# Kernel tuning notes

Hardware: AMD Instinct MI355X
Metric: run time of the kernel (lower is better)

The kernel has to match this reference:

```python
import jax, jax.numpy as jnp
import numpy as np

D = 1024
H = 16
HD = D // H


def setup_inputs() -> dict:
    key = jax.random.key(0)
    ks = jax.random.split(key, 11)
    B, S = 4, 1024
    s = 0.02
    return {
        "q": jax.random.normal(ks[0], (B, S, D), jnp.float32),
        "k": jax.random.normal(ks[1], (B, S, D), jnp.float32),
        "v": jax.random.normal(ks[2], (B, S, D), jnp.float32),
        "Wq": jax.random.normal(ks[3], (D, D), jnp.float32) * s,
        "bq": jnp.zeros((D,), jnp.float32),
        "Wk": jax.random.normal(ks[4], (D, D), jnp.float32) * s,
        "bk": jnp.zeros((D,), jnp.float32),
        "Wv": jax.random.normal(ks[5], (D, D), jnp.float32) * s,
        "bv": jnp.zeros((D,), jnp.float32),
        "Wo": jax.random.normal(ks[6], (D, D), jnp.float32) * s,
        "bo": jnp.zeros((D,), jnp.float32),
    }


def _split_heads(x):
    # [B, S, D] -> [B, H, S, HD]
    B, S, _ = x.shape
    return x.reshape(B, S, H, HD).transpose(0, 2, 1, 3)


def reference(q, k, v, Wq, bq, Wk, bk, Wv, bv, Wo, bo):
    # Projections followed by ReLU (faithful to the original module)
    qh = _split_heads(jax.nn.relu(q @ Wq + bq))
    kh = _split_heads(jax.nn.relu(k @ Wk + bk))
    vh = _split_heads(jax.nn.relu(v @ Wv + bv))
    # NOTE: original scales by sqrt(input_dim), not sqrt(head_dim)
    scale = 1.0 / jnp.sqrt(jnp.float32(D))
    scores = jnp.einsum("bhsd,bhtd->bhst", qh, kh) * scale  # [B,H,S,S]
    weights = jax.nn.softmax(scores, axis=-1)  # dropout is identity in eval
    attn = jnp.einsum("bhst,bhtd->bhsd", weights, vh)  # [B,H,S,HD]
    B, _, S, _ = attn.shape
    attn = attn.transpose(0, 2, 1, 3).reshape(B, S, D)
    return attn @ Wo + bo
```

## Files before the change

### kernel.cpp

```cpp
#include <hip/hip_runtime.h>
#include <math.h>

#define Dm 1024
#define Hn 16
#define HDn 64
#define Sn 1024

typedef __attribute__((ext_vector_type(8))) __bf16 bf16x8;
typedef __attribute__((ext_vector_type(4))) float floatx4;

__device__ __forceinline__ void async_ld16(void* lds, const void* g) {
    __builtin_amdgcn_global_load_lds(
        (const __attribute__((address_space(1))) void*)g,
        (__attribute__((address_space(3))) void*)lds,
        16, 0, 0);
}

struct PrepArgs {
    const float* qkv[3];
    __bf16*      qkv_o[3];
    const float* W[4];
    __bf16*      WT[4];
    float*       out_zero;
};

__global__ __launch_bounds__(256) void prep_kernel(PrepArgs a)
{
    __shared__ float sT[64][65];
    const int z = blockIdx.z, x = blockIdx.x, tid = threadIdx.x;

    if (z < 3) {
        const float* src = a.qkv[z];
        __bf16* dst = a.qkv_o[z];
        const int lin = x * 256 + tid;
        const float4 v0 = ((const float4*)src)[lin * 2];
        const float4 v1 = ((const float4*)src)[lin * 2 + 1];
        bf16x8 o;
        o[0] = (__bf16)v0.x; o[1] = (__bf16)v0.y; o[2] = (__bf16)v0.z; o[3] = (__bf16)v0.w;
        o[4] = (__bf16)v1.x; o[5] = (__bf16)v1.y; o[6] = (__bf16)v1.z; o[7] = (__bf16)v1.w;
        ((bf16x8*)dst)[lin] = o;
    } else if (z < 7) {
        if (x >= 256) return;
        const float* W = a.W[z - 3];
        __bf16* O = a.WT[z - 3];
        const int bi = (x >> 4) * 64, bj = (x & 15) * 64;
        const int colr = tid & 63, rowg = tid >> 6;
        #pragma unroll
        for (int i = 0; i < 16; ++i) {
            const int kk = i * 4 + rowg;
            sT[kk][colr] = W[(size_t)(bi + kk) * Dm + bj + colr];
        }
        __syncthreads();
        #pragma unroll
        for (int i = 0; i < 16; ++i) {
            const int rn = i * 4 + rowg;
            O[(size_t)(bj + rn) * Dm + bi + colr] = (__bf16)sT[colr][rn];
        }
    } else {
        float4* o = (float4*)a.out_zero;
        const int i = (x * 256 + tid) * 2;
        const float4 zz = make_float4(0.f, 0.f, 0.f, 0.f);
        o[i] = zz;
        o[i + 1] = zz;
    }
}

struct GemmArgs {
    const __bf16* X[3];
    const __bf16* WT[3];
    const float*  bias[3];
    void*         out[3];
    int   layout[3];
    float esc[3];
};

__global__ __launch_bounds__(256) void gemm_bf16_kernel(GemmArgs args)
{
    __shared__ __align__(16) __bf16 sA[128 * 32];
    __shared__ __align__(16) __bf16 sB[128 * 32];

    const int z = blockIdx.z;
    const __bf16* __restrict__ Xb  = args.X[z];
    const __bf16* __restrict__ WTb = args.WT[z];
    const float*  __restrict__ bias = args.bias[z];
    void* __restrict__ outp = args.out[z];
    const int layout = args.layout[z];
    const float escale = args.esc[z];

    const int tid = threadIdx.x;
    const int id = blockIdx.x + (blockIdx.y << 3);
    const int bm = (((id & 7) << 2) | (id >> 6)) * 128;
    const int bn = ((id >> 3) & 7) * 128;

    const int lane = tid & 63;
    const int wave = tid >> 6;
    const int wm = (wave & 1) * 64;
    const int wn = (wave >> 1) * 64;
    const int l15 = lane & 15, quad = lane >> 4;

    floatx4 acc[4][4];
    #pragma unroll
    for (int mi = 0; mi < 4; ++mi)
        #pragma unroll
        for (int ni = 0; ni < 4; ++ni)
            acc[mi][ni] = (floatx4){0.f, 0.f, 0.f, 0.f};

    const int cA0 = tid,       p0 = cA0 >> 3, g0 = (cA0 & 7) ^ (p0 & 7);
    const int cA1 = tid + 256, p1 = cA1 >> 3, g1 = (cA1 & 7) ^ (p1 & 7);
    const int r0 = 2 * p0 + (g0 >> 2), q0 = g0 & 3;
    const int r1 = 2 * p1 + (g1 >> 2), q1 = g1 & 3;
    const __bf16* gA0 = Xb  + (size_t)(bm + r0) * Dm + q0 * 8;
    const __bf16* gA1 = Xb  + (size_t)(bm + r1) * Dm + q1 * 8;
    const __bf16* gB0 = WTb + (size_t)(bn + r0) * Dm + q0 * 8;
    const __bf16* gB1 = WTb + (size_t)(bn + r1) * Dm + q1 * 8;
    char* const lA0 = (char*)sA + (tid & 192) * 16;
    char* const lA1 = (char*)sA + (256 + (tid & 192)) * 16;
    char* const lB0 = (char*)sB + (tid & 192) * 16;
    char* const lB1 = (char*)sB + (256 + (tid & 192)) * 16;

    int offA[4], offB[4];
    #pragma unroll
    for (int mi = 0; mi < 4; ++mi) {
        const int r = wm + mi * 16 + l15;
        const int p = r >> 1;
        const int cc = ((((r & 1) << 2) | quad)) ^ (p & 7);
        offA[mi] = p * 64 + cc * 8;
    }
    #pragma unroll
    for (int ni = 0; ni < 4; ++ni) {
        const int r = wn + ni * 16 + l15;
        const int p = r >> 1;
        const int cc = ((((r & 1) << 2) | quad)) ^ (p & 7);
        offB[ni] = p * 64 + cc * 8;
    }

    for (int kt = 0; kt < Dm; kt += 32) {
        async_ld16(lA0, gA0 + kt);
        async_ld16(lA1, gA1 + kt);
        async_ld16(lB0, gB0 + kt);
        async_ld16(lB1, gB1 + kt);
        __syncthreads();

        bf16x8 af[4], bfr[4];
        #pragma unroll
        for (int mi = 0; mi < 4; ++mi) af[mi] = *(const bf16x8*)(sA + offA[mi]);
        #pragma unroll
        for (int ni = 0; ni < 4; ++ni) bfr[ni] = *(const bf16x8*)(sB + offB[ni]);
        #pragma unroll
        for (int mi = 0; mi < 4; ++mi)
            #pragma unroll
            for (int ni = 0; ni < 4; ++ni)
                acc[mi][ni] = __builtin_amdgcn_mfma_f32_16x16x32_bf16(
                    af[mi], bfr[ni], acc[mi][ni], 0, 0, 0);
        __syncthreads();
    }

    #pragma unroll
    for (int mi = 0; mi < 4; ++mi) {
        #pragma unroll
        for (int ni = 0; ni < 4; ++ni) {
            const int n = bn + wn + ni * 16 + l15;
            const float bv = bias[n];
            const int h = n >> 6, d = n & 63;
            #pragma unroll
            for (int reg = 0; reg < 4; ++reg) {
                const int m = bm + wm + mi * 16 + quad * 4 + reg;
                const int b = m >> 10, s = m & 1023;
                float v = fmaxf(acc[mi][ni][reg] + bv, 0.0f) * escale;
                if (layout == 0)
                    ((__bf16*)outp)[((size_t)(b * Hn + h) * 1024 + s) * 64 + d] = (__bf16)v;
                else
                    ((__bf16*)outp)[((size_t)(b * Hn + h) * 64 + d) * 1024 + s] = (__bf16)v;
            }
        }
    }
}

__global__ __launch_bounds__(256) void gemm_splitk_kernel(
    const __bf16* __restrict__ Xb, const __bf16* __restrict__ WTb,
    const float* __restrict__ bias, float* __restrict__ outp)
{
    __shared__ __align__(16) __bf16 sA[128 * 64];
    __shared__ __align__(16) __bf16 sB[128 * 64];

    const int tid = threadIdx.x;
    const int kz = blockIdx.z;
    const int id = blockIdx.x + (blockIdx.y << 3);
    const int bm = (((id & 7) << 2) | (id >> 6)) * 128;
    const int bn = ((id >> 3) & 7) * 128;

    const int lane = tid & 63;
    const int wave = tid >> 6;
    const int wm = (wave & 1) * 64;
    const int wn = (wave >> 1) * 64;
    const int l15 = lane & 15, quad = lane >> 4;

    floatx4 acc[4][4];
    #pragma unroll
    for (int mi = 0; mi < 4; ++mi)
        #pragma unroll
        for (int ni = 0; ni < 4; ++ni)
            acc[mi][ni] = (floatx4){0.f, 0.f, 0.f, 0.f};

    const int kofs = kz * 512;
    const __bf16* gA[4];
    const __bf16* gB[4];
    #pragma unroll
    for (int j = 0; j < 4; ++j) {
        const int c = j * 256 + tid;
        const int row = c >> 3;
        const int q = (c & 7) ^ (row & 7);
        gA[j] = Xb  + (size_t)(bm + row) * Dm + kofs + q * 8;
        gB[j] = WTb + (size_t)(bn + row) * Dm + kofs + q * 8;
    }
    char* const lA = (char*)sA + (tid & 192) * 16;
    char* const lB = (char*)sB + (tid & 192) * 16;

    for (int kt = 0; kt < 512; kt += 64) {
        #pragma unroll
        for (int j = 0; j < 4; ++j) {
            async_ld16(lA + j * 4096, gA[j] + kt);
            async_ld16(lB + j * 4096, gB[j] + kt);
        }
        __syncthreads();

        #pragma unroll
        for (int ks = 0; ks < 2; ++ks) {
            bf16x8 af[4], bfr[4];
            #pragma unroll
            for (int mi = 0; mi < 4; ++mi) {
                const int r = wm + mi * 16 + l15;
                af[mi] = *(const bf16x8*)(sA + r * 64 + ((((ks << 2) + quad) ^ (r & 7)) * 8));
            }
            #pragma unroll
            for (int ni = 0; ni < 4; ++ni) {
                const int r = wn + ni * 16 + l15;
                bfr[ni] = *(const bf16x8*)(sB + r * 64 + ((((ks << 2) + quad) ^ (r & 7)) * 8));
            }
            #pragma unroll
            for (int mi = 0; mi < 4; ++mi)
                #pragma unroll
                for (int ni = 0; ni < 4; ++ni)
                    acc[mi][ni] = __builtin_amdgcn_mfma_f32_16x16x32_bf16(
                        af[mi], bfr[ni], acc[mi][ni], 0, 0, 0);
        }
        __syncthreads();
    }

    #pragma unroll
    for (int mi = 0; mi < 4; ++mi) {
        #pragma unroll
        for (int ni = 0; ni < 4; ++ni) {
            const int n = bn + wn + ni * 16 + l15;
            const float bv = (kz == 0) ? bias[n] : 0.0f;
            #pragma unroll
            for (int reg = 0; reg < 4; ++reg) {
                const int m = bm + wm + mi * 16 + quad * 4 + reg;
                atomicAdd(outp + (size_t)m * 1024 + n, acc[mi][ni][reg] + bv);
            }
        }
    }
}

__global__ __launch_bounds__(256, 2) void flash_attn_kernel(
    const __bf16* __restrict__ Qh,
    const __bf16* __restrict__ Kh,
    const __bf16* __restrict__ Vt,
    __bf16* __restrict__ ctx)
{
    __shared__ __align__(16) char sKV[2][16384];
    __shared__ __align__(16) __bf16 sP[4][32 * 64];

    const int tid = threadIdx.x;
    const int wave = tid >> 6, lane = tid & 63;
    const int l15 = lane & 15, quad = lane >> 4;

    const int id = blockIdx.x + (blockIdx.y << 3) + (blockIdx.z << 7);
    const int kk = id >> 3;
    const int bh = ((id & 7) << 3) | (kk & 7);
    const int b = bh >> 4, h = bh & 15;
    const int qb = (kk >> 3) * 128 + wave * 32;

    bf16x8 aQ[2][2];
    #pragma unroll
    for (int mi = 0; mi < 2; ++mi)
        #pragma unroll
        for (int ks = 0; ks < 2; ++ks)
            aQ[mi][ks] = *(const bf16x8*)(Qh +
                (size_t)(bh * Sn + qb + mi * 16 + l15) * 64 + ks * 32 + quad * 8);

    const int s0 = tid, s1 = tid + 256;
    const int r0 = s0 >> 3, q0c = (s0 & 7) ^ (r0 & 7);
    const int r1 = s1 >> 3, q1c = (s1 & 7) ^ (r1 & 7);
    const __bf16* gK0 = Kh + (size_t)(bh * Sn + r0) * 64 + q0c * 8;
    const __bf16* gK1 = Kh + (size_t)(bh * Sn + r1) * 64 + q1c * 8;
    const __bf16* gV0 = Vt + (size_t)(bh * 64 + r0) * Sn + q0c * 8;
    const __bf16* gV1 = Vt + (size_t)(bh * 64 + r1) * Sn + q1c * 8;
    const int wofs = (tid & 192) * 16;

    floatx4 oacc[2][4];
    #pragma unroll
    for (int mi = 0; mi < 2; ++mi)
        #pragma unroll
        for (int nf = 0; nf < 4; ++nf)
            oacc[mi][nf] = (floatx4){0.f, 0.f, 0.f, 0.f};
    float lsum[2][4];
    #pragma unroll
    for (int mi = 0; mi < 2; ++mi)
        #pragma unroll
        for (int r = 0; r < 4; ++r) lsum[mi][r] = 0.0f;

    __bf16* sPw = sP[wave];

    {
        char* bK = sKV[0];
        char* bV = sKV[0] + 8192;
        async_ld16(bK + wofs,        gK0);
        async_ld16(bK + 4096 + wofs, gK1);
        async_ld16(bV + wofs,        gV0);
        async_ld16(bV + 4096 + wofs, gV1);
    }

    int cur = 0;
    for (int it = 0; it < 16; ++it) {
        __syncthreads();

        if (it + 1 < 16) {
            const int t0n = (it + 1) * 64;
            char* bK = sKV[cur ^ 1];
            char* bV = sKV[cur ^ 1] + 8192;
            async_ld16(bK + wofs,        gK0 + (size_t)t0n * 64);
            async_ld16(bK + 4096 + wofs, gK1 + (size_t)t0n * 64);
            async_ld16(bV + wofs,        gV0 + t0n);
            async_ld16(bV + 4096 + wofs, gV1 + t0n);
        }

        const __bf16* sK = (const __bf16*)sKV[cur];
        const __bf16* sV = (const __bf16*)(sKV[cur] + 8192);

        floatx4 sc[2][4];
        #pragma unroll
        for (int mi = 0; mi < 2; ++mi)
            #pragma unroll
            for (int nf = 0; nf < 4; ++nf)
                sc[mi][nf] = (floatx4){0.f, 0.f, 0.f, 0.f};
        #pragma unroll
        for (int ks = 0; ks < 2; ++ks) {
            bf16x8 bK[4];
            #pragma unroll
            for (int nf = 0; nf < 4; ++nf) {
                const int n = nf * 16 + l15;
                bK[nf] = *(const bf16x8*)(sK + (n * 8 + (((ks << 2) + quad) ^ (n & 7))) * 8);
            }
            #pragma unroll
            for (int mi = 0; mi < 2; ++mi)
                #pragma unroll
                for (int nf = 0; nf < 4; ++nf)
                    sc[mi][nf] = __builtin_amdgcn_mfma_f32_16x16x32_bf16(
                        aQ[mi][ks], bK[nf], sc[mi][nf], 0, 0, 0);
        }

        #pragma unroll
        for (int mi = 0; mi < 2; ++mi)
            #pragma unroll
            for (int nf = 0; nf < 4; ++nf) {
                const int t = nf * 16 + l15;
                #pragma unroll
                for (int r = 0; r < 4; ++r) {
                    const float p = __builtin_amdgcn_exp2f(fminf(sc[mi][nf][r], 126.0f));
                    const __bf16 pb = (__bf16)p;
                    lsum[mi][r] += (float)pb;
                    const int rr = mi * 16 + quad * 4 + r;
                    sPw[(rr * 8 + ((t >> 3) ^ (rr & 7))) * 8 + (t & 7)] = pb;
                }
            }

        #pragma unroll
        for (int ks = 0; ks < 2; ++ks) {
            bf16x8 aP[2], bV[4];
            #pragma unroll
            for (int mi = 0; mi < 2; ++mi) {
                const int r = mi * 16 + l15;
                aP[mi] = *(const bf16x8*)(sPw + (r * 8 + (((ks << 2) + quad) ^ (r & 7))) * 8);
            }
            #pragma unroll
            for (int nf = 0; nf < 4; ++nf) {
                const int n = nf * 16 + l15;
                bV[nf] = *(const bf16x8*)(sV + (n * 8 + (((ks << 2) + quad) ^ (n & 7))) * 8);
            }
            #pragma unroll
            for (int mi = 0; mi < 2; ++mi)
                #pragma unroll
                for (int nf = 0; nf < 4; ++nf)
                    oacc[mi][nf] = __builtin_amdgcn_mfma_f32_16x16x32_bf16(
                        aP[mi], bV[nf], oacc[mi][nf], 0, 0, 0);
        }

        cur ^= 1;
    }

    float linv[2][4];
    #pragma unroll
    for (int mi = 0; mi < 2; ++mi)
        #pragma unroll
        for (int r = 0; r < 4; ++r) {
            float l = lsum[mi][r];
            l += __shfl_xor(l, 1, 64);
            l += __shfl_xor(l, 2, 64);
            l += __shfl_xor(l, 4, 64);
            l += __shfl_xor(l, 8, 64);
            linv[mi][r] = 1.0f / l;
        }

    #pragma unroll
    for (int mi = 0; mi < 2; ++mi)
        #pragma unroll
        for (int nf = 0; nf < 4; ++nf) {
            const int d = h * 64 + nf * 16 + l15;
            #pragma unroll
            for (int reg = 0; reg < 4; ++reg) {
                const int s = qb + mi * 16 + quad * 4 + reg;
                ctx[(size_t)(b * Sn + s) * Dm + d] =
                    (__bf16)(oacc[mi][nf][reg] * linv[mi][reg]);
            }
        }
}

extern "C" void kernel_launch(void* const* d_in, const int* in_sizes, int n_in,
                              void* d_out, int out_size, void* d_ws, size_t ws_size,
                              hipStream_t stream)
{
    const float* q  = (const float*)d_in[0];
    const float* k  = (const float*)d_in[1];
    const float* v  = (const float*)d_in[2];
    const float* Wq = (const float*)d_in[3];
    const float* bq = (const float*)d_in[4];
    const float* Wk = (const float*)d_in[5];
    const float* bk = (const float*)d_in[6];
    const float* Wv = (const float*)d_in[7];
    const float* bv = (const float*)d_in[8];
    const float* Wo = (const float*)d_in[9];
    const float* bo = (const float*)d_in[10];

    char* ws = (char*)d_ws;
    const size_t MB = 1024 * 1024;
    __bf16* qb_ = (__bf16*)(ws);
    __bf16* kb_ = (__bf16*)(ws + 8 * MB);
    __bf16* vb_ = (__bf16*)(ws + 16 * MB);
    __bf16* WTq = (__bf16*)(ws + 24 * MB);
    __bf16* WTk = (__bf16*)(ws + 26 * MB);
    __bf16* WTv = (__bf16*)(ws + 28 * MB);
    __bf16* WTo = (__bf16*)(ws + 30 * MB);
    __bf16* Qh  = (__bf16*)(ws + 32 * MB);
    __bf16* Kh  = (__bf16*)(ws + 40 * MB);
    __bf16* Vt  = (__bf16*)(ws + 48 * MB);
    __bf16* ctx = (__bf16*)(ws + 56 * MB);

    PrepArgs pa;
    pa.qkv[0] = q; pa.qkv[1] = k; pa.qkv[2] = v;
    pa.qkv_o[0] = qb_; pa.qkv_o[1] = kb_; pa.qkv_o[2] = vb_;
    pa.W[0] = Wq; pa.W[1] = Wk; pa.W[2] = Wv; pa.W[3] = Wo;
    pa.WT[0] = WTq; pa.WT[1] = WTk; pa.WT[2] = WTv; pa.WT[3] = WTo;
    pa.out_zero = (float*)d_out;
    prep_kernel<<<dim3(2048, 1, 8), 256, 0, stream>>>(pa);

    const float QSCALE = 0.0450842200f;

    GemmArgs qkv;
    qkv.X[0] = qb_;  qkv.X[1] = kb_;  qkv.X[2] = vb_;
    qkv.WT[0] = WTq; qkv.WT[1] = WTk; qkv.WT[2] = WTv;
    qkv.bias[0] = bq; qkv.bias[1] = bk; qkv.bias[2] = bv;
    qkv.out[0] = Qh;  qkv.out[1] = Kh;  qkv.out[2] = Vt;
    qkv.layout[0] = 0; qkv.layout[1] = 0; qkv.layout[2] = 1;
    qkv.esc[0] = QSCALE; qkv.esc[1] = 1.0f; qkv.esc[2] = 1.0f;
    gemm_bf16_kernel<<<dim3(8, 32, 3), 256, 0, stream>>>(qkv);

    flash_attn_kernel<<<dim3(8, 16, 4), 256, 0, stream>>>(Qh, Kh, Vt, ctx);

    gemm_splitk_kernel<<<dim3(8, 32, 2), 256, 0, stream>>>(
        ctx, WTo, bo, (float*)d_out);
}
```

Baseline: 224.6 us.

## Replace atomic split-K output GEMM with in-block LDS reduction; halve QKV tile M

The output projection no longer splits K across two blocks with atomicAdd into a pre-zeroed buffer. Instead each 512-thread block runs both K halves in separate wave groups and reduces them through LDS before a plain store, which also removes the zeroing pass from the prep kernel. Separately, the QKV GEMM tile height drops from 128 to 64 rows, doubling the grid for better CU occupancy at the cost of less B-tile reuse. The output kernel now needs 64KB of LDS per block and an extra block-wide sync.

```diff
diff --git a/kernel.cpp b/kernel.cpp
--- a/kernel.cpp
+++ b/kernel.cpp
@@ -21,7 +21,6 @@
     __bf16*      qkv_o[3];
     const float* W[4];
     __bf16*      WT[4];
-    float*       out_zero;
 };
 
 __global__ __launch_bounds__(256) void prep_kernel(PrepArgs a)
@@ -39,7 +38,7 @@
         o[0] = (__bf16)v0.x; o[1] = (__bf16)v0.y; o[2] = (__bf16)v0.z; o[3] = (__bf16)v0.w;
         o[4] = (__bf16)v1.x; o[5] = (__bf16)v1.y; o[6] = (__bf16)v1.z; o[7] = (__bf16)v1.w;
         ((bf16x8*)dst)[lin] = o;
-    } else if (z < 7) {
+    } else {
         if (x >= 256) return;
         const float* W = a.W[z - 3];
         __bf16* O = a.WT[z - 3];
@@ -56,12 +55,6 @@
             const int rn = i * 4 + rowg;
             O[(size_t)(bj + rn) * Dm + bi + colr] = (__bf16)sT[colr][rn];
         }
-    } else {
-        float4* o = (float4*)a.out_zero;
-        const int i = (x * 256 + tid) * 2;
-        const float4 zz = make_float4(0.f, 0.f, 0.f, 0.f);
-        o[i] = zz;
-        o[i + 1] = zz;
     }
 }
 
@@ -76,7 +69,7 @@
 
 __global__ __launch_bounds__(256) void gemm_bf16_kernel(GemmArgs args)
 {
-    __shared__ __align__(16) __bf16 sA[128 * 32];
+    __shared__ __align__(16) __bf16 sA[64 * 32];
     __shared__ __align__(16) __bf16 sB[128 * 32];
 
     const int z = blockIdx.z;
@@ -89,38 +82,38 @@
 
     const int tid = threadIdx.x;
     const int id = blockIdx.x + (blockIdx.y << 3);
-    const int bm = (((id & 7) << 2) | (id >> 6)) * 128;
+    const int bm = (((id & 7) << 3) | (id >> 6)) * 64;
     const int bn = ((id >> 3) & 7) * 128;
 
     const int lane = tid & 63;
     const int wave = tid >> 6;
-    const int wm = (wave & 1) * 64;
+    const int wm = (wave & 1) * 32;
     const int wn = (wave >> 1) * 64;
     const int l15 = lane & 15, quad = lane >> 4;
 
-    floatx4 acc[4][4];
-    #pragma unroll
-    for (int mi = 0; mi < 4; ++mi)
+    floatx4 acc[2][4];
+    #pragma unroll
+    for (int mi = 0; mi < 2; ++mi)
         #pragma unroll
         for (int ni = 0; ni < 4; ++ni)
             acc[mi][ni] = (floatx4){0.f, 0.f, 0.f, 0.f};
 
-    const int cA0 = tid,       p0 = cA0 >> 3, g0 = (cA0 & 7) ^ (p0 & 7);
-    const int cA1 = tid + 256, p1 = cA1 >> 3, g1 = (cA1 & 7) ^ (p1 & 7);
-    const int r0 = 2 * p0 + (g0 >> 2), q0 = g0 & 3;
-    const int r1 = 2 * p1 + (g1 >> 2), q1 = g1 & 3;
-    const __bf16* gA0 = Xb  + (size_t)(bm + r0) * Dm + q0 * 8;
-    const __bf16* gA1 = Xb  + (size_t)(bm + r1) * Dm + q1 * 8;
-    const __bf16* gB0 = WTb + (size_t)(bn + r0) * Dm + q0 * 8;
-    const __bf16* gB1 = WTb + (size_t)(bn + r1) * Dm + q1 * 8;
+    const int cA = tid, pA = cA >> 3, gAx = (cA & 7) ^ (pA & 7);
+    const int rA = 2 * pA + (gAx >> 2), qA = gAx & 3;
+    const __bf16* gA0 = Xb + (size_t)(bm + rA) * Dm + qA * 8;
+    const int cB0 = tid,       pB0 = cB0 >> 3, gB0x = (cB0 & 7) ^ (pB0 & 7);
+    const int cB1 = tid + 256, pB1 = cB1 >> 3, gB1x = (cB1 & 7) ^ (pB1 & 7);
+    const int rB0 = 2 * pB0 + (gB0x >> 2), qB0 = gB0x & 3;
+    const int rB1 = 2 * pB1 + (gB1x >> 2), qB1 = gB1x & 3;
+    const __bf16* gB0p = WTb + (size_t)(bn + rB0) * Dm + qB0 * 8;
+    const __bf16* gB1p = WTb + (size_t)(bn + rB1) * Dm + qB1 * 8;
     char* const lA0 = (char*)sA + (tid & 192) * 16;
-    char* const lA1 = (char*)sA + (256 + (tid & 192)) * 16;
     char* const lB0 = (char*)sB + (tid & 192) * 16;
     char* const lB1 = (char*)sB + (256 + (tid & 192)) * 16;
 
-    int offA[4], offB[4];
-    #pragma unroll
-    for (int mi = 0; mi < 4; ++mi) {
+    int offA[2], offB[4];
+    #pragma unroll
+    for (int mi = 0; mi < 2; ++mi) {
         const int r = wm + mi * 16 + l15;
         const int p = r >> 1;
         const int cc = ((((r & 1) << 2) | quad)) ^ (p & 7);
@@ -136,18 +129,17 @@
 
     for (int kt = 0; kt < Dm; kt += 32) {
         async_ld16(lA0, gA0 + kt);
-        async_ld16(lA1, gA1 + kt);
-        async_ld16(lB0, gB0 + kt);
-        async_ld16(lB1, gB1 + kt);
-        __syncthreads();
-
-        bf16x8 af[4], bfr[4];
-        #pragma unroll
-        for (int mi = 0; mi < 4; ++mi) af[mi] = *(const bf16x8*)(sA + offA[mi]);
+        async_ld16(lB0, gB0p + kt);
+        async_ld16(lB1, gB1p + kt);
+        __syncthreads();
+
+        bf16x8 af[2], bfr[4];
+        #pragma unroll
+        for (int mi = 0; mi < 2; ++mi) af[mi] = *(const bf16x8*)(sA + offA[mi]);
         #pragma unroll
         for (int ni = 0; ni < 4; ++ni) bfr[ni] = *(const bf16x8*)(sB + offB[ni]);
         #pragma unroll
-        for (int mi = 0; mi < 4; ++mi)
+        for (int mi = 0; mi < 2; ++mi)
             #pragma unroll
             for (int ni = 0; ni < 4; ++ni)
                 acc[mi][ni] = __builtin_amdgcn_mfma_f32_16x16x32_bf16(
@@ -156,7 +148,7 @@
     }
 
     #pragma unroll
-    for (int mi = 0; mi < 4; ++mi) {
+    for (int mi = 0; mi < 2; ++mi) {
         #pragma unroll
         for (int ni = 0; ni < 4; ++ni) {
             const int n = bn + wn + ni * 16 + l15;
@@ -176,23 +168,25 @@
     }
 }
 
-__global__ __launch_bounds__(256) void gemm_splitk_kernel(
+__global__ __launch_bounds__(512) void gemm_out_kernel(
     const __bf16* __restrict__ Xb, const __bf16* __restrict__ WTb,
     const float* __restrict__ bias, float* __restrict__ outp)
 {
-    __shared__ __align__(16) __bf16 sA[128 * 64];
-    __shared__ __align__(16) __bf16 sB[128 * 64];
-
-    const int tid = threadIdx.x;
-    const int kz = blockIdx.z;
+    __shared__ __align__(16) __bf16 sA[2][128 * 64];
+    __shared__ __align__(16) __bf16 sB[2][128 * 64];
+
+    const int tid  = threadIdx.x;
+    const int half = tid >> 8;
+    const int tidh = tid & 255;
     const int id = blockIdx.x + (blockIdx.y << 3);
     const int bm = (((id & 7) << 2) | (id >> 6)) * 128;
     const int bn = ((id >> 3) & 7) * 128;
 
     const int lane = tid & 63;
     const int wave = tid >> 6;
-    const int wm = (wave & 1) * 64;
-    const int wn = (wave >> 1) * 64;
+    const int wave4 = wave & 3;
+    const int wm = (wave4 & 1) * 64;
+    const int wn = (wave4 >> 1) * 64;
     const int l15 = lane & 15, quad = lane >> 4;
 
     floatx4 acc[4][4];
@@ -202,19 +196,21 @@
         for (int ni = 0; ni < 4; ++ni)
             acc[mi][ni] = (floatx4){0.f, 0.f, 0.f, 0.f};
 
-    const int kofs = kz * 512;
+    const int kofs = half * 512;
     const __bf16* gA[4];
     const __bf16* gB[4];
     #pragma unroll
     for (int j = 0; j < 4; ++j) {
-        const int c = j * 256 + tid;
+        const int c = j * 256 + tidh;
         const int row = c >> 3;
         const int q = (c & 7) ^ (row & 7);
         gA[j] = Xb  + (size_t)(bm + row) * Dm + kofs + q * 8;
         gB[j] = WTb + (size_t)(bn + row) * Dm + kofs + q * 8;
     }
-    char* const lA = (char*)sA + (tid & 192) * 16;
-    char* const lB = (char*)sB + (tid & 192) * 16;
+    char* const lA = (char*)(&sA[half][0]) + (tidh & 192) * 16;
+    char* const lB = (char*)(&sB[half][0]) + (tidh & 192) * 16;
+    const __bf16* const rdA = &sA[half][0];
+    const __bf16* const rdB = &sB[half][0];
 
     for (int kt = 0; kt < 512; kt += 64) {
         #pragma unroll
@@ -230,12 +226,12 @@
             #pragma unroll
             for (int mi = 0; mi < 4; ++mi) {
                 const int r = wm + mi * 16 + l15;
-                af[mi] = *(const bf16x8*)(sA + r * 64 + ((((ks << 2) + quad) ^ (r & 7)) * 8));
+                af[mi] = *(const bf16x8*)(rdA + r * 64 + ((((ks << 2) + quad) ^ (r & 7)) * 8));
             }
             #pragma unroll
             for (int ni = 0; ni < 4; ++ni) {
                 const int r = wn + ni * 16 + l15;
-                bfr[ni] = *(const bf16x8*)(sB + r * 64 + ((((ks << 2) + quad) ^ (r & 7)) * 8));
+                bfr[ni] = *(const bf16x8*)(rdB + r * 64 + ((((ks << 2) + quad) ^ (r & 7)) * 8));
             }
             #pragma unroll
             for (int mi = 0; mi < 4; ++mi)
@@ -247,16 +243,33 @@
         __syncthreads();
     }
 
-    #pragma unroll
-    for (int mi = 0; mi < 4; ++mi) {
-        #pragma unroll
-        for (int ni = 0; ni < 4; ++ni) {
-            const int n = bn + wn + ni * 16 + l15;
-            const float bv = (kz == 0) ? bias[n] : 0.0f;
-            #pragma unroll
-            for (int reg = 0; reg < 4; ++reg) {
-                const int m = bm + wm + mi * 16 + quad * 4 + reg;
-                atomicAdd(outp + (size_t)m * 1024 + n, acc[mi][ni][reg] + bv);
+    if (half == 1) {
+        floatx4* scratch = (wave < 6)
+            ? (floatx4*)(&sA[0][0]) + (wave - 4) * 1024
+            : (floatx4*)(&sB[0][0]) + (wave - 6) * 1024;
+        #pragma unroll
+        for (int mi = 0; mi < 4; ++mi)
+            #pragma unroll
+            for (int ni = 0; ni < 4; ++ni)
+                scratch[(mi * 4 + ni) * 64 + lane] = acc[mi][ni];
+    }
+    __syncthreads();
+    if (half == 0) {
+        const floatx4* scratch = (wave < 2)
+            ? (const floatx4*)(&sA[0][0]) + wave * 1024
+            : (const floatx4*)(&sB[0][0]) + (wave - 2) * 1024;
+        #pragma unroll
+        for (int mi = 0; mi < 4; ++mi) {
+            #pragma unroll
+            for (int ni = 0; ni < 4; ++ni) {
+                const floatx4 other = scratch[(mi * 4 + ni) * 64 + lane];
+                const int n = bn + wn + ni * 16 + l15;
+                const float bv = bias[n];
+                #pragma unroll
+                for (int reg = 0; reg < 4; ++reg) {
+                    const int m = bm + wm + mi * 16 + quad * 4 + reg;
+                    outp[(size_t)m * 1024 + n] = (acc[mi][ni][reg] + other[reg]) + bv;
+                }
             }
         }
     }
@@ -461,8 +474,7 @@
     pa.qkv_o[0] = qb_; pa.qkv_o[1] = kb_; pa.qkv_o[2] = vb_;
     pa.W[0] = Wq; pa.W[1] = Wk; pa.W[2] = Wv; pa.W[3] = Wo;
     pa.WT[0] = WTq; pa.WT[1] = WTk; pa.WT[2] = WTv; pa.WT[3] = WTo;
-    pa.out_zero = (float*)d_out;
-    prep_kernel<<<dim3(2048, 1, 8), 256, 0, stream>>>(pa);
+    prep_kernel<<<dim3(2048, 1, 7), 256, 0, stream>>>(pa);
 
     const float QSCALE = 0.0450842200f;
 
@@ -473,10 +485,10 @@
     qkv.out[0] = Qh;  qkv.out[1] = Kh;  qkv.out[2] = Vt;
     qkv.layout[0] = 0; qkv.layout[1] = 0; qkv.layout[2] = 1;
     qkv.esc[0] = QSCALE; qkv.esc[1] = 1.0f; qkv.esc[2] = 1.0f;
-    gemm_bf16_kernel<<<dim3(8, 32, 3), 256, 0, stream>>>(qkv);
+    gemm_bf16_kernel<<<dim3(8, 64, 3), 256, 0, stream>>>(qkv);
 
     flash_attn_kernel<<<dim3(8, 16, 4), 256, 0, stream>>>(Qh, Kh, Vt, ctx);
 
-    gemm_splitk_kernel<<<dim3(8, 32, 2), 256, 0, stream>>>(
+    gemm_out_kernel<<<dim3(8, 32, 1), 512, 0, stream>>>(
         ctx, WTo, bo, (float*)d_out);
 }
```

Result: faster. 218.5 us (-2.7%).
